# Performance work log

Measured on AMD Instinct MI355X. Metric: run time of the kernel, lower is better.

The kernel has to match this reference:

```python
import jax, jax.numpy as jnp
import numpy as np

N_NODES = 100000
N_EDGES = 1600000
D_IN = 64
D_OUT = 64


def setup_inputs() -> dict:
    key = jax.random.key(0)
    k1, k2, k3, k4, k5, k6 = jax.random.split(key, 6)
    feat = jax.random.normal(k1, (N_NODES, D_IN), dtype=jnp.float32)
    src = jax.random.randint(k2, (N_EDGES,), 0, N_NODES, dtype=jnp.int64)
    dst = jax.random.randint(k3, (N_EDGES,), 0, N_NODES, dtype=jnp.int64)
    edge_weight = jax.random.uniform(k4, (N_EDGES,), dtype=jnp.float32)
    # Xavier-uniform with relu gain, as in reset_parameters
    gain = float(np.sqrt(2.0))
    bound = gain * float(np.sqrt(6.0 / (D_IN + D_OUT)))
    W_neigh = jax.random.uniform(k5, (D_OUT, D_IN), dtype=jnp.float32, minval=-bound, maxval=bound)
    W_self = jax.random.uniform(k6, (D_OUT, D_IN), dtype=jnp.float32, minval=-bound, maxval=bound)
    bias = jnp.zeros((D_OUT,), dtype=jnp.float32)
    return {"feat": feat, "src": src, "dst": dst, "edge_weight": edge_weight,
            "W_neigh": W_neigh, "W_self": W_self, "bias": bias}


def reference(feat, src, dst, edge_weight, W_neigh, W_self, bias):
    n = feat.shape[0]
    # feat_drop with p=0.0 is identity; in_feats == out_feats so lin_before_mp is False
    # message: u_mul_e -> gather src features, scale by edge weight  [E, D_IN]
    m = feat[src] * edge_weight[:, None]
    # mean reduce over incoming edges (zero for isolated dst nodes, matching DGL)
    s = jax.ops.segment_sum(m, dst, num_segments=n)
    deg = jax.ops.segment_sum(jnp.ones_like(edge_weight), dst, num_segments=n)
    neigh = s / jnp.maximum(deg, 1.0)[:, None]
    h_neigh = neigh @ W_neigh.T
    h_self = feat @ W_self.T
    return h_self + h_neigh + bias
```

## Files before the change

kernel.cpp:

```cpp
#include <hip/hip_runtime.h>

constexpr int N_NODES = 100000;
constexpr int N_EDGES = 1600000;
constexpr int D = 64;

constexpr int BSH    = 6;
constexpr int BN     = 1 << BSH;
constexpr int NBUCK  = (N_NODES + BN - 1) / BN;
constexpr int NPART  = 200;
constexpr int EPB    = N_EDGES / NPART;
constexpr int CAP    = 2048;
constexpr int NCVT   = (N_NODES * D / 4) / 256;

constexpr size_t OFF_BCNT    = 0;
constexpr size_t OFF_CURSOR  = 8192;
constexpr size_t OFF_BSTART  = 16384;
constexpr size_t OFF_ENTRIES = 24576;
constexpr size_t OFF_W16     = 24576 + (size_t)N_EDGES * 8;
constexpr size_t OFF_FEAT16  = 12845056;
constexpr size_t WS_NEEDED   = OFF_FEAT16 + (size_t)N_NODES * D * 2;

typedef short  bf16x8 __attribute__((ext_vector_type(8)));
typedef float  f32x4  __attribute__((ext_vector_type(4)));

union FragU { unsigned u[4]; bf16x8 v; };

__device__ __forceinline__ unsigned short f2bf(float f) {
    unsigned u = __float_as_uint(f);
    u += 0x7fffu + ((u >> 16) & 1u);
    return (unsigned short)(u >> 16);
}

__global__ __launch_bounds__(256) void k_zero(int* __restrict__ bcnt) {
    int i = blockIdx.x * 256 + threadIdx.x;
    if (i < NBUCK) bcnt[i] = 0;
}

__global__ __launch_bounds__(256) void k_pre(const float4* __restrict__ feat4,
                                             unsigned short* __restrict__ feat16,
                                             const float* __restrict__ Wn,
                                             const float* __restrict__ Ws,
                                             unsigned short* __restrict__ W16,
                                             const int* __restrict__ dst,
                                             int* __restrict__ bcnt) {
    __shared__ int l[NBUCK];
    const int b   = blockIdx.x;
    const int tid = threadIdx.x;
    if (b < NCVT) {
        const int i = b * 256 + tid;
        float4 v = feat4[i];
        ushort4 o;
        o.x = f2bf(v.x); o.y = f2bf(v.y); o.z = f2bf(v.z); o.w = f2bf(v.w);
        *(ushort4*)&feat16[(size_t)i * 4] = o;
    } else if (b < NCVT + NPART) {
        const int base = (b - NCVT) * EPB;
        for (int i = tid; i < NBUCK; i += 256) l[i] = 0;
        __syncthreads();
        for (int k = tid; k < EPB; k += 256)
            atomicAdd(&l[dst[base + k] >> BSH], 1);
        __syncthreads();
        for (int i = tid; i < NBUCK; i += 256)
            if (l[i]) atomicAdd(&bcnt[i], l[i]);
    } else {
        for (int e = tid; e < D * 128; e += 256) {
            const int j = e >> 7, k = e & 127;
            const float w = (k < D) ? Ws[j * D + k] : Wn[j * D + (k - D)];
            W16[e] = f2bf(w);
        }
    }
}

__global__ __launch_bounds__(1024) void k_scan(const int* __restrict__ bcnt,
                                               int* __restrict__ bstart,
                                               int* __restrict__ cursor) {
    __shared__ int s[1024];
    const int t  = threadIdx.x;
    const int i0 = 2 * t, i1 = 2 * t + 1;
    const int c0 = (i0 < NBUCK) ? bcnt[i0] : 0;
    const int c1 = (i1 < NBUCK) ? bcnt[i1] : 0;
    const int v  = c0 + c1;
    s[t] = v;
    __syncthreads();
    for (int off = 1; off < 1024; off <<= 1) {
        int u = (t >= off) ? s[t - off] : 0;
        __syncthreads();
        s[t] += u;
        __syncthreads();
    }
    const int excl = s[t] - v;
    if (i0 < NBUCK) { bstart[i0] = excl;      cursor[i0] = excl; }
    if (i1 < NBUCK) { bstart[i1] = excl + c0; cursor[i1] = excl + c0; }
    if (t == 0) bstart[NBUCK] = N_EDGES;
}

__global__ __launch_bounds__(256) void k_part(const int* __restrict__ src,
                                              const int* __restrict__ dst,
                                              const float* __restrict__ ew,
                                              int* __restrict__ cursor,
                                              uint2* __restrict__ entries) {
    __shared__ int l[NBUCK];
    const int tid  = threadIdx.x;
    const int base = blockIdx.x * EPB;
    for (int i = tid; i < NBUCK; i += 256) l[i] = 0;
    __syncthreads();
    for (int k = tid; k < EPB; k += 256)
        atomicAdd(&l[dst[base + k] >> BSH], 1);
    __syncthreads();
    for (int b = tid; b < NBUCK; b += 256) {
        const int c = l[b];
        l[b] = c ? atomicAdd(&cursor[b], c) : 0;
    }
    __syncthreads();
    for (int k = tid; k < EPB; k += 256) {
        const int e = base + k;
        const int d = dst[e];
        const int pos = atomicAdd(&l[d >> BSH], 1);
        entries[pos] = make_uint2((unsigned)src[e] | ((unsigned)(d & (BN - 1)) << 17),
                                  __float_as_uint(ew[e]));
    }
}

__global__ __launch_bounds__(256) void k_bucket(const uint2* __restrict__ feat16u2,
                                                const unsigned short* __restrict__ feat16,
                                                const int* __restrict__ bstart,
                                                const uint2* __restrict__ entries,
                                                const unsigned short* __restrict__ W16,
                                                const float* __restrict__ bias,
                                                float* __restrict__ out) {
    __shared__ uint2 ent[CAP];
    __shared__ __align__(16) uint2 aggrow[BN * 16];
    __shared__ int hh[BN], st[BN], cur[BN];
    const int tid = threadIdx.x;
    const int b   = blockIdx.x;
    const int s0  = bstart[b];
    int cnt = bstart[b + 1] - s0;
    if (cnt > CAP) cnt = CAP;

    if (tid < BN) hh[tid] = 0;
    __syncthreads();
    for (int i = tid; i < cnt; i += 256)
        atomicAdd(&hh[(entries[s0 + i].x >> 17) & (BN - 1)], 1);
    __syncthreads();
    if (tid < BN) st[tid] = hh[tid];
    __syncthreads();
    for (int off = 1; off < BN; off <<= 1) {
        int u = 0;
        if (tid < BN && tid >= off) u = st[tid - off];
        __syncthreads();
        if (tid < BN) st[tid] += u;
        __syncthreads();
    }
    if (tid < BN) { const int e0 = st[tid] - hh[tid]; st[tid] = e0; cur[tid] = e0; }
    __syncthreads();
    for (int i = tid; i < cnt; i += 256) {
        uint2 e = entries[s0 + i];
        const int pos = atomicAdd(&cur[(e.x >> 17) & (BN - 1)], 1);
        ent[pos] = e;
    }
    __syncthreads();

    const int wave = tid >> 6, lane = tid & 63;
    const int group = lane >> 4, gl = lane & 15;
    for (int t = 0; t < 16; ++t) {
        const int dl  = wave * 16 + t;
        const int ss  = st[dl];
        const int deg = hh[dl];
        const int se  = ss + deg;
        float4 acc = make_float4(0.f, 0.f, 0.f, 0.f);
        for (int e = ss + group; e < se; e += 4) {
            const uint2 en = ent[e];
            const float w  = __uint_as_float(en.y);
            const uint2 p  = feat16u2[(size_t)(en.x & 0x1FFFF) * 16 + gl];
            acc.x = fmaf(__uint_as_float(p.x << 16),         w, acc.x);
            acc.y = fmaf(__uint_as_float(p.x & 0xFFFF0000u), w, acc.y);
            acc.z = fmaf(__uint_as_float(p.y << 16),         w, acc.z);
            acc.w = fmaf(__uint_as_float(p.y & 0xFFFF0000u), w, acc.w);
        }
#pragma unroll
        for (int m = 16; m <= 32; m <<= 1) {
            acc.x += __shfl_xor(acc.x, m);
            acc.y += __shfl_xor(acc.y, m);
            acc.z += __shfl_xor(acc.z, m);
            acc.w += __shfl_xor(acc.w, m);
        }
        if (group == 0) {
            const float inv = 1.0f / fmaxf((float)deg, 1.0f);
            uint2 o;
            o.x = (unsigned)f2bf(acc.x * inv) | ((unsigned)f2bf(acc.y * inv) << 16);
            o.y = (unsigned)f2bf(acc.z * inv) | ((unsigned)f2bf(acc.w * inv) << 16);
            aggrow[dl * 16 + gl] = o;
        }
    }
    __syncthreads();

    const int quad = lane >> 4, r = lane & 15;
    const int node0 = b * BN + wave * 16;
    int arow = node0 + r;
    if (arow > N_NODES - 1) arow = N_NODES - 1;

    bf16x8 a[4], bb[4][4];
    a[0] = *(const bf16x8*)&feat16[(size_t)arow * 64 +      quad * 8];
    a[1] = *(const bf16x8*)&feat16[(size_t)arow * 64 + 32 + quad * 8];
    {
        const int rbase = (wave * 16 + r) * 16;
        FragU f2, f3;
        uint2 lo = aggrow[rbase + 2 * quad];
        uint2 hi = aggrow[rbase + 2 * quad + 1];
        f2.u[0] = lo.x; f2.u[1] = lo.y; f2.u[2] = hi.x; f2.u[3] = hi.y;
        lo = aggrow[rbase + 8 + 2 * quad];
        hi = aggrow[rbase + 8 + 2 * quad + 1];
        f3.u[0] = lo.x; f3.u[1] = lo.y; f3.u[2] = hi.x; f3.u[3] = hi.y;
        a[2] = f2.v;
        a[3] = f3.v;
    }
#pragma unroll
    for (int nt = 0; nt < 4; ++nt)
#pragma unroll
        for (int kc = 0; kc < 4; ++kc)
            bb[nt][kc] = *(const bf16x8*)&W16[(size_t)(nt * 16 + r) * 128 + kc * 32 + quad * 8];

    f32x4 acc[4] = {};
#pragma unroll
    for (int kc = 0; kc < 4; ++kc)
#pragma unroll
        for (int nt = 0; nt < 4; ++nt)
            acc[nt] = __builtin_amdgcn_mfma_f32_16x16x32_bf16(a[kc], bb[nt][kc], acc[nt], 0, 0, 0);

#pragma unroll
    for (int nt = 0; nt < 4; ++nt) {
        const float bv = bias[nt * 16 + r];
#pragma unroll
        for (int reg = 0; reg < 4; ++reg) {
            const int m = node0 + quad * 4 + reg;
            if (m < N_NODES) out[(size_t)m * 64 + nt * 16 + r] = acc[nt][reg] + bv;
        }
    }
}

__global__ __launch_bounds__(256) void fb_zero(float4* __restrict__ out4,
                                               float* __restrict__ deg) {
    const int stride = gridDim.x * blockDim.x;
    int i = blockIdx.x * blockDim.x + threadIdx.x;
    const int total4 = (N_NODES * D) / 4;
    for (int idx = i; idx < total4; idx += stride)
        out4[idx] = make_float4(0.f, 0.f, 0.f, 0.f);
    for (int idx = i; idx < N_NODES; idx += stride)
        deg[idx] = 0.f;
}

__global__ __launch_bounds__(256) void fb_scatter(
    const float* __restrict__ feat, const int* __restrict__ src,
    const int* __restrict__ dst, const float* __restrict__ ew,
    float* __restrict__ out, float* __restrict__ deg) {
    const int gid  = blockIdx.x * blockDim.x + threadIdx.x;
    const int e    = gid >> 6;
    const int lane = gid & 63;
    if (e >= N_EDGES) return;
    atomicAdd(&out[(size_t)dst[e] * D + lane], feat[(size_t)src[e] * D + lane] * ew[e]);
    if (lane == 0) atomicAdd(&deg[dst[e]], 1.0f);
}

__global__ __launch_bounds__(256) void fb_finalize(
    const float* __restrict__ feat, const float* __restrict__ Wn,
    const float* __restrict__ Ws, const float* __restrict__ bias,
    const float* __restrict__ deg, float* __restrict__ out) {
    __shared__ float lWn[D * 65];
    __shared__ float lWs[D * 65];
    for (int idx = threadIdx.x; idx < D * D; idx += 256) {
        const int r = idx >> 6, c = idx & 63;
        lWn[r * 65 + c] = Wn[idx];
        lWs[r * 65 + c] = Ws[idx];
    }
    __syncthreads();
    const int wave = threadIdx.x >> 6;
    const int lane = threadIdx.x & 63;
    const int n = blockIdx.x * 4 + wave;
    if (n >= N_NODES) return;
    const float f  = feat[(size_t)n * D + lane];
    const float sv = out[(size_t)n * D + lane];
    const float inv = 1.0f / fmaxf(deg[n], 1.0f);
    float acc_s = 0.f, acc_n = 0.f;
#pragma unroll
    for (int k = 0; k < D; ++k) {
        acc_s += __shfl(f, k)  * lWs[lane * 65 + k];
        acc_n += __shfl(sv, k) * lWn[lane * 65 + k];
    }
    out[(size_t)n * D + lane] = acc_s + acc_n * inv + bias[lane];
}

extern "C" void kernel_launch(void* const* d_in, const int* in_sizes, int n_in,
                              void* d_out, int out_size, void* d_ws, size_t ws_size,
                              hipStream_t stream) {
    const float* feat = (const float*)d_in[0];
    const int*   src  = (const int*)  d_in[1];
    const int*   dst  = (const int*)  d_in[2];
    const float* ew   = (const float*)d_in[3];
    const float* Wn   = (const float*)d_in[4];
    const float* Ws   = (const float*)d_in[5];
    const float* bias = (const float*)d_in[6];
    float* out = (float*)d_out;
    char* ws = (char*)d_ws;

    if (ws_size >= WS_NEEDED) {
        int*   bcnt    = (int*)(ws + OFF_BCNT);
        int*   cursor  = (int*)(ws + OFF_CURSOR);
        int*   bstart  = (int*)(ws + OFF_BSTART);
        uint2* entries = (uint2*)(ws + OFF_ENTRIES);
        unsigned short* W16    = (unsigned short*)(ws + OFF_W16);
        unsigned short* feat16 = (unsigned short*)(ws + OFF_FEAT16);

        k_zero  <<<(NBUCK + 255) / 256, 256, 0, stream>>>(bcnt);
        k_pre   <<<NCVT + NPART + 1, 256, 0, stream>>>((const float4*)feat, feat16,
                                                       Wn, Ws, W16, dst, bcnt);
        k_scan  <<<1, 1024, 0, stream>>>(bcnt, bstart, cursor);
        k_part  <<<NPART, 256, 0, stream>>>(src, dst, ew, cursor, entries);
        k_bucket<<<NBUCK, 256, 0, stream>>>((const uint2*)feat16, feat16, bstart,
                                            entries, W16, bias, out);
    } else {
        float* deg = (float*)d_ws;
        fb_zero<<<2048, 256, 0, stream>>>((float4*)out, deg);
        fb_scatter<<<(N_EDGES * 64) / 256, 256, 0, stream>>>(feat, src, dst, ew, out, deg);
        fb_finalize<<<(N_NODES + 3) / 4, 256, 0, stream>>>(feat, Wn, Ws, bias, deg, out);
    }
}
```

Measured before the change: 234.3 us.

## Replace counting-sort scan with fixed-capacity bucket slabs and per-node rank atomics

Removes the histogram pass in k_pre and the single-block scan kernel. Each bucket now writes into a fixed CAP-sized slab in workspace, and per-node global atomic counters assign each edge a rank that is packed into the entry. k_bucket can then place entries directly in shared memory without a local histogram or LDS atomics. This costs one extra global atomic per edge and a larger, sparser entries buffer, and it silently drops edges beyond CAP per bucket or RMAX per node.

```diff
diff --git a/kernel.cpp b/kernel.cpp
--- a/kernel.cpp
+++ b/kernel.cpp
@@ -10,14 +10,14 @@
 constexpr int NPART  = 200;
 constexpr int EPB    = N_EDGES / NPART;
 constexpr int CAP    = 2048;
+constexpr int RMAX   = 512;
 constexpr int NCVT   = (N_NODES * D / 4) / 256;
 
-constexpr size_t OFF_BCNT    = 0;
-constexpr size_t OFF_CURSOR  = 8192;
-constexpr size_t OFF_BSTART  = 16384;
-constexpr size_t OFF_ENTRIES = 24576;
-constexpr size_t OFF_W16     = 24576 + (size_t)N_EDGES * 8;
-constexpr size_t OFF_FEAT16  = 12845056;
+constexpr size_t OFF_NCUR    = 0;
+constexpr size_t OFF_BCUR    = 400000;
+constexpr size_t OFF_W16     = 409600;
+constexpr size_t OFF_ENTRIES = 425984;
+constexpr size_t OFF_FEAT16  = 26034176;
 constexpr size_t WS_NEEDED   = OFF_FEAT16 + (size_t)N_NODES * D * 2;
 
 typedef short  bf16x8 __attribute__((ext_vector_type(8)));
@@ -31,19 +31,20 @@
     return (unsigned short)(u >> 16);
 }
 
-__global__ __launch_bounds__(256) void k_zero(int* __restrict__ bcnt) {
-    int i = blockIdx.x * 256 + threadIdx.x;
-    if (i < NBUCK) bcnt[i] = 0;
+__global__ __launch_bounds__(256) void k_zero(int* __restrict__ ncur,
+                                              int* __restrict__ bcur) {
+    const int stride = gridDim.x * 256;
+    for (int i = blockIdx.x * 256 + threadIdx.x; i < N_NODES; i += stride)
+        ncur[i] = 0;
+    for (int i = blockIdx.x * 256 + threadIdx.x; i < NBUCK; i += stride)
+        bcur[i] = 0;
 }
 
 __global__ __launch_bounds__(256) void k_pre(const float4* __restrict__ feat4,
                                              unsigned short* __restrict__ feat16,
                                              const float* __restrict__ Wn,
                                              const float* __restrict__ Ws,
-                                             unsigned short* __restrict__ W16,
-                                             const int* __restrict__ dst,
-                                             int* __restrict__ bcnt) {
-    __shared__ int l[NBUCK];
+                                             unsigned short* __restrict__ W16) {
     const int b   = blockIdx.x;
     const int tid = threadIdx.x;
     if (b < NCVT) {
@@ -52,15 +53,6 @@
         ushort4 o;
         o.x = f2bf(v.x); o.y = f2bf(v.y); o.z = f2bf(v.z); o.w = f2bf(v.w);
         *(ushort4*)&feat16[(size_t)i * 4] = o;
-    } else if (b < NCVT + NPART) {
-        const int base = (b - NCVT) * EPB;
-        for (int i = tid; i < NBUCK; i += 256) l[i] = 0;
-        __syncthreads();
-        for (int k = tid; k < EPB; k += 256)
-            atomicAdd(&l[dst[base + k] >> BSH], 1);
-        __syncthreads();
-        for (int i = tid; i < NBUCK; i += 256)
-            if (l[i]) atomicAdd(&bcnt[i], l[i]);
     } else {
         for (int e = tid; e < D * 128; e += 256) {
             const int j = e >> 7, k = e & 127;
@@ -70,33 +62,11 @@
     }
 }
 
-__global__ __launch_bounds__(1024) void k_scan(const int* __restrict__ bcnt,
-                                               int* __restrict__ bstart,
-                                               int* __restrict__ cursor) {
-    __shared__ int s[1024];
-    const int t  = threadIdx.x;
-    const int i0 = 2 * t, i1 = 2 * t + 1;
-    const int c0 = (i0 < NBUCK) ? bcnt[i0] : 0;
-    const int c1 = (i1 < NBUCK) ? bcnt[i1] : 0;
-    const int v  = c0 + c1;
-    s[t] = v;
-    __syncthreads();
-    for (int off = 1; off < 1024; off <<= 1) {
-        int u = (t >= off) ? s[t - off] : 0;
-        __syncthreads();
-        s[t] += u;
-        __syncthreads();
-    }
-    const int excl = s[t] - v;
-    if (i0 < NBUCK) { bstart[i0] = excl;      cursor[i0] = excl; }
-    if (i1 < NBUCK) { bstart[i1] = excl + c0; cursor[i1] = excl + c0; }
-    if (t == 0) bstart[NBUCK] = N_EDGES;
-}
-
 __global__ __launch_bounds__(256) void k_part(const int* __restrict__ src,
                                               const int* __restrict__ dst,
                                               const float* __restrict__ ew,
-                                              int* __restrict__ cursor,
+                                              int* __restrict__ ncur,
+                                              int* __restrict__ bcur,
                                               uint2* __restrict__ entries) {
     __shared__ int l[NBUCK];
     const int tid  = threadIdx.x;
@@ -108,38 +78,43 @@
     __syncthreads();
     for (int b = tid; b < NBUCK; b += 256) {
         const int c = l[b];
-        l[b] = c ? atomicAdd(&cursor[b], c) : 0;
+        l[b] = c ? atomicAdd(&bcur[b], c) : 0;
     }
     __syncthreads();
     for (int k = tid; k < EPB; k += 256) {
         const int e = base + k;
         const int d = dst[e];
-        const int pos = atomicAdd(&l[d >> BSH], 1);
-        entries[pos] = make_uint2((unsigned)src[e] | ((unsigned)(d & (BN - 1)) << 17),
-                                  __float_as_uint(ew[e]));
+        const int bk = d >> BSH;
+        const int pos = atomicAdd(&l[bk], 1);
+        const int r   = atomicAdd(&ncur[d], 1);
+        if (pos < CAP && r < RMAX)
+            entries[(size_t)bk * CAP + pos] =
+                make_uint2((unsigned)src[e] | ((unsigned)(d & (BN - 1)) << 17)
+                                            | ((unsigned)r << 23),
+                           __float_as_uint(ew[e]));
     }
 }
 
 __global__ __launch_bounds__(256) void k_bucket(const uint2* __restrict__ feat16u2,
                                                 const unsigned short* __restrict__ feat16,
-                                                const int* __restrict__ bstart,
+                                                const int* __restrict__ ncur,
+                                                const int* __restrict__ bcur,
                                                 const uint2* __restrict__ entries,
                                                 const unsigned short* __restrict__ W16,
                                                 const float* __restrict__ bias,
                                                 float* __restrict__ out) {
     __shared__ uint2 ent[CAP];
     __shared__ __align__(16) uint2 aggrow[BN * 16];
-    __shared__ int hh[BN], st[BN], cur[BN];
+    __shared__ int hh[BN], st[BN];
     const int tid = threadIdx.x;
     const int b   = blockIdx.x;
-    const int s0  = bstart[b];
-    int cnt = bstart[b + 1] - s0;
+    int cnt = bcur[b];
     if (cnt > CAP) cnt = CAP;
 
-    if (tid < BN) hh[tid] = 0;
-    __syncthreads();
-    for (int i = tid; i < cnt; i += 256)
-        atomicAdd(&hh[(entries[s0 + i].x >> 17) & (BN - 1)], 1);
+    if (tid < BN) {
+        const int node = b * BN + tid;
+        hh[tid] = (node < N_NODES) ? ncur[node] : 0;
+    }
     __syncthreads();
     if (tid < BN) st[tid] = hh[tid];
     __syncthreads();
@@ -150,12 +125,14 @@
         if (tid < BN) st[tid] += u;
         __syncthreads();
     }
-    if (tid < BN) { const int e0 = st[tid] - hh[tid]; st[tid] = e0; cur[tid] = e0; }
-    __syncthreads();
+    if (tid < BN) st[tid] -= hh[tid];
+    __syncthreads();
+    const uint2* slab = entries + (size_t)b * CAP;
     for (int i = tid; i < cnt; i += 256) {
-        uint2 e = entries[s0 + i];
-        const int pos = atomicAdd(&cur[(e.x >> 17) & (BN - 1)], 1);
-        ent[pos] = e;
+        const uint2 e = slab[i];
+        const int dl = (e.x >> 17) & (BN - 1);
+        const int r  = (int)(e.x >> 23);
+        ent[st[dl] + r] = e;
     }
     __syncthreads();
 
@@ -302,19 +279,16 @@
     char* ws = (char*)d_ws;
 
     if (ws_size >= WS_NEEDED) {
-        int*   bcnt    = (int*)(ws + OFF_BCNT);
-        int*   cursor  = (int*)(ws + OFF_CURSOR);
-        int*   bstart  = (int*)(ws + OFF_BSTART);
+        int*   ncur    = (int*)(ws + OFF_NCUR);
+        int*   bcur    = (int*)(ws + OFF_BCUR);
         uint2* entries = (uint2*)(ws + OFF_ENTRIES);
         unsigned short* W16    = (unsigned short*)(ws + OFF_W16);
         unsigned short* feat16 = (unsigned short*)(ws + OFF_FEAT16);
 
-        k_zero  <<<(NBUCK + 255) / 256, 256, 0, stream>>>(bcnt);
-        k_pre   <<<NCVT + NPART + 1, 256, 0, stream>>>((const float4*)feat, feat16,
-                                                       Wn, Ws, W16, dst, bcnt);
-        k_scan  <<<1, 1024, 0, stream>>>(bcnt, bstart, cursor);
-        k_part  <<<NPART, 256, 0, stream>>>(src, dst, ew, cursor, entries);
-        k_bucket<<<NBUCK, 256, 0, stream>>>((const uint2*)feat16, feat16, bstart,
+        k_zero  <<<128, 256, 0, stream>>>(ncur, bcur);
+        k_pre   <<<NCVT + 1, 256, 0, stream>>>((const float4*)feat, feat16, Wn, Ws, W16);
+        k_part  <<<NPART, 256, 0, stream>>>(src, dst, ew, ncur, bcur, entries);
+        k_bucket<<<NBUCK, 256, 0, stream>>>((const uint2*)feat16, feat16, ncur, bcur,
                                             entries, W16, bias, out);
     } else {
         float* deg = (float*)d_ws;
```

After: 282.7 us. 20.6% more time.
